# Performance work log

Measured on AMD Instinct MI355X. Metric: run time of the kernel, lower is better.

## Reference

```python
import jax, jax.numpy as jnp
import numpy as np

B, T, D_MODEL, H = 2, 2048, 1024, 16
D_HEAD = D_MODEL // H


def setup_inputs() -> dict:
    key = jax.random.key(0)
    k1, k2, k3 = jax.random.split(key, 3)
    x = jax.random.normal(k1, (B, T, D_MODEL), dtype=jnp.float32)
    # Linear weights stored as (in, out); scale like torch default init roughly
    W_qkv = jax.random.normal(k2, (D_MODEL, 3 * D_MODEL), dtype=jnp.float32) / np.sqrt(D_MODEL)
    W_o = jax.random.normal(k3, (D_MODEL, D_MODEL), dtype=jnp.float32) / np.sqrt(D_MODEL)
    return {"x": x, "W_qkv": W_qkv, "W_o": W_o}


def reference(x, W_qkv, W_o):
    Bx, Tx, C = x.shape
    qkv = x @ W_qkv                                   # (B,T,3C)
    qkv = qkv.reshape(Bx, Tx, 3, H, D_HEAD)
    q = qkv[:, :, 0].transpose(0, 2, 1, 3)            # (B,H,T,D)
    k = qkv[:, :, 1].transpose(0, 2, 1, 3)
    v = qkv[:, :, 2].transpose(0, 2, 1, 3)
    scale = 1.0 / np.sqrt(D_HEAD).astype(np.float32)
    att = jnp.einsum('bhqd,bhkd->bhqk', q, k) * scale  # (B,H,T,T)
    causal = jnp.tril(jnp.ones((Tx, Tx), dtype=bool))
    att = jnp.where(causal[None, None], att, jnp.float32(-jnp.inf))
    w = jax.nn.softmax(att, axis=-1)
    out = jnp.einsum('bhqk,bhkd->bhqd', w, v)          # (B,H,T,D)
    out = out.transpose(0, 2, 1, 3).reshape(Bx, Tx, C)
    return out @ W_o
```

## Files before the change

### kernel.cpp

```cpp
#include <hip/hip_runtime.h>

typedef unsigned short u16;
typedef unsigned int u32;
typedef __bf16 bf16x8 __attribute__((ext_vector_type(8)));
typedef float f32x4 __attribute__((ext_vector_type(4)));

#define DEV __device__ __forceinline__

constexpr int BB = 2;
constexpr int TT = 2048;
constexpr int CD = 1024;
constexpr int HH = 16;
constexpr int DH = 64;
constexpr int BT = BB * TT;

#define QSCALE 0.18033688011112042f

DEV u16 f2bf(float f) {
    return __builtin_bit_cast(u16, (__bf16)f);
}

DEV f32x4 mfma16(bf16x8 a, bf16x8 b, f32x4 c) {
    return __builtin_amdgcn_mfma_f32_16x16x32_bf16(a, b, c, 0, 0, 0);
}

DEV void gld_lds16(u16* lds, const u16* g) {
    __builtin_amdgcn_global_load_lds(
        (const __attribute__((address_space(1))) unsigned int*)g,
        (__attribute__((address_space(3))) unsigned int*)lds, 16, 0, 0);
}

__global__ __launch_bounds__(256)
void prep_kernel(const float* __restrict__ x, u16* __restrict__ xb,
                 const float* __restrict__ Wqkv, u16* __restrict__ WqkvT,
                 const float* __restrict__ Wo, u16* __restrict__ WoT) {
    const int tid = threadIdx.x;
    int blk = blockIdx.x;
    if (blk < 2048) {
        const int i = (blk * 256 + tid) * 8;
        float4 a = *(const float4*)&x[i];
        float4 b = *(const float4*)&x[i + 4];
        u16 t[8];
        t[0] = f2bf(a.x); t[1] = f2bf(a.y); t[2] = f2bf(a.z); t[3] = f2bf(a.w);
        t[4] = f2bf(b.x); t[5] = f2bf(b.y); t[6] = f2bf(b.z); t[7] = f2bf(b.w);
        *(uint4*)&xb[i] = *(const uint4*)t;
        return;
    }
    __shared__ u16 tile[64][72];
    const float* in; u16* out; int rows, cols, bx, by;
    blk -= 2048;
    if (blk < 768) { in = Wqkv; out = WqkvT; rows = 1024; cols = 3072; bx = blk % 48; by = blk / 48; }
    else { blk -= 768; in = Wo; out = WoT; rows = 1024; cols = 1024; bx = blk % 16; by = blk / 16; }
    const int c0 = bx * 64, r0 = by * 64;

    const int tx = tid & 15, ty = tid >> 4;
    #pragma unroll
    for (int p = 0; p < 4; ++p) {
        const int r = ty + p * 16;
        float4 v = *(const float4*)&in[(size_t)(r0 + r) * cols + c0 + tx * 4];
        tile[tx * 4 + 0][r] = f2bf(v.x);
        tile[tx * 4 + 1][r] = f2bf(v.y);
        tile[tx * 4 + 2][r] = f2bf(v.z);
        tile[tx * 4 + 3][r] = f2bf(v.w);
    }
    __syncthreads();

    const int c = tid >> 2, r8 = (tid & 3) * 16;
    u16* dst = &out[(size_t)(c0 + c) * rows + r0 + r8];
    *(uint4*)dst       = *(const uint4*)&tile[c][r8];
    *(uint4*)(dst + 8) = *(const uint4*)&tile[c][r8 + 8];
}

template <int EPI, int BM, int BN, int GX>
__global__ __launch_bounds__(256)
void gemm_db(const u16* __restrict__ A, const u16* __restrict__ Bt,
             u16* __restrict__ out0, u16* __restrict__ out1,
             u16* __restrict__ out2, float* __restrict__ outf,
             int M, int N, int K) {
    constexpr int BK = 32, AST = 32;
    constexpr int MT = BM / 32;
    constexpr int NT = BN / 32;
    constexpr int MBLK = 4096 / BM;
    constexpr int NBLK = GX * MBLK;
    constexpr int CPX = NBLK / 8;
    constexpr int LPS = BM / 64 + BN / 64;
    __shared__ alignas(16) u16 As[3][BM * AST];
    __shared__ alignas(16) u16 Bs[3][BN * AST];

    const int tid  = threadIdx.x;
    const int wave = tid >> 6, lane = tid & 63;
    const int quad = lane >> 4, l16 = lane & 15;
    const int wm = (wave & 1) * (BM / 2), wn = (wave >> 1) * (BN / 2);

    int bid = (int)blockIdx.x;
    bid = (bid & 7) * CPX + (bid >> 3);
    const int bx = bid % GX, by = bid / GX;
    const int m0 = by * BM, n0 = bx * BN;

    const int srowA = wave * (BM / 4) + (lane >> 2);
    const int srowB = wave * (BN / 4) + (lane >> 2);
    const int scol  = (((lane & 3) ^ ((lane >> 3) & 3))) * 8;
    const u16* ga0 = A  + (size_t)(m0 + srowA) * K + scol;
    const u16* ga1 = ga0 + (size_t)16 * K;
    const u16* gb0 = Bt + (size_t)(n0 + srowB) * K + scol;
    const u16* gb1 = gb0 + (size_t)16 * K;

    auto stage = [&](int buf, int k0) {
        gld_lds16(&As[buf][wave * (BM / 4) * 32],       ga0 + k0);
        if constexpr (BM == 128)
            gld_lds16(&As[buf][wave * (BM / 4) * 32 + 512], ga1 + k0);
        gld_lds16(&Bs[buf][wave * (BN / 4) * 32],       gb0 + k0);
        if constexpr (BN == 128)
            gld_lds16(&Bs[buf][wave * (BN / 4) * 32 + 512], gb1 + k0);
    };
    auto wait_lps = [&]() {
        if constexpr (LPS == 4)      asm volatile("s_waitcnt vmcnt(4)" ::: "memory");
        else if constexpr (LPS == 3) asm volatile("s_waitcnt vmcnt(3)" ::: "memory");
        else                         asm volatile("s_waitcnt vmcnt(2)" ::: "memory");
    };

    f32x4 acc[MT][NT] = {};

    stage(0, 0);
    stage(1, BK);
    wait_lps();
    __builtin_amdgcn_s_barrier();

    const int sx = ((l16 >> 1) & 3) * 8;
    const int NS = K / BK;
    int cb = 0;
    for (int t = 0; t < NS; ++t) {
        const bool pf = (t + 2 < NS);
        int sb = cb + 2; if (sb >= 3) sb -= 3;
        if (pf) stage(sb, (t + 2) * BK);

        bf16x8 fa[MT], fb[NT];
        #pragma unroll
        for (int mt = 0; mt < MT; ++mt)
            fa[mt] = *(const bf16x8*)
                &As[cb][(wm + mt * 16 + l16) * AST + (quad * 8 ^ sx)];
        #pragma unroll
        for (int nt = 0; nt < NT; ++nt)
            fb[nt] = *(const bf16x8*)
                &Bs[cb][(wn + nt * 16 + l16) * AST + (quad * 8 ^ sx)];
        #pragma unroll
        for (int mt = 0; mt < MT; ++mt)
            #pragma unroll
            for (int nt = 0; nt < NT; ++nt)
                acc[mt][nt] = mfma16(fa[mt], fb[nt], acc[mt][nt]);

        if (pf) wait_lps();
        else    asm volatile("s_waitcnt vmcnt(0)" ::: "memory");
        __builtin_amdgcn_s_barrier();
        cb = (cb + 1 == 3) ? 0 : cb + 1;
    }

    #pragma unroll
    for (int mt = 0; mt < MT; ++mt) {
        #pragma unroll
        for (int nt = 0; nt < NT; ++nt) {
            #pragma unroll
            for (int reg = 0; reg < 4; ++reg) {
                const int r = m0 + wm + mt * 16 + quad * 4 + reg;
                const int c = n0 + wn + nt * 16 + l16;
                if (EPI == 0) {
                    outf[(size_t)r * N + c] = acc[mt][nt][reg];
                } else {
                    const int which = c >> 10;
                    const int cc = c & 1023;
                    const int h = cc >> 6, d = cc & 63;
                    const int b = r >> 11, t = r & 2047;
                    const int bh = b * HH + h;
                    if (which == 0) {
                        out0[((size_t)bh * TT + t) * DH + d] =
                            f2bf(acc[mt][nt][reg] * QSCALE);
                    } else if (which == 1) {
                        out1[((size_t)bh * TT + t) * DH + d] = f2bf(acc[mt][nt][reg]);
                    } else {
                        out2[((size_t)bh * DH + d) * TT + t] = f2bf(acc[mt][nt][reg]);
                    }
                }
            }
        }
    }
}

constexpr int KST = 72;

DEV void attn_step(const bf16x8 fk[4][2], const bf16x8 fv[2][4],
                   const bf16x8 fone, const bf16x8* fq,
                   f32x4* Oacc, f32x4& lacc, float& m_i, bool diag,
                   int wave, int quad, int l16) {
    f32x4 st[4];
    #pragma unroll
    for (int nt = 0; nt < 4; ++nt) {
        f32x4 t = {};
        t = mfma16(fk[nt][0], fq[0], t);
        t = mfma16(fk[nt][1], fq[1], t);
        st[nt] = t;
    }

    if (diag) {
        const int qg = wave * 16 + l16;
        #pragma unroll
        for (int nt = 0; nt < 4; ++nt)
            #pragma unroll
            for (int reg = 0; reg < 4; ++reg) {
                const int kg = nt * 16 + quad * 4 + reg;
                st[nt][reg] = (kg <= qg) ? st[nt][reg] : -INFINITY;
            }
    }

    float v[16];
    #pragma unroll
    for (int nt = 0; nt < 4; ++nt)
        #pragma unroll
        for (int reg = 0; reg < 4; ++reg)
            v[nt * 4 + reg] = st[nt][reg];
    #pragma unroll
    for (int s = 8; s > 0; s >>= 1)
        #pragma unroll
        for (int i = 0; i < s; ++i)
            v[i] = fmaxf(v[i], v[i + s]);
    float vmax = v[0];
    vmax = fmaxf(vmax, __shfl_xor(vmax, 16, 64));
    vmax = fmaxf(vmax, __shfl_xor(vmax, 32, 64));

    if (!__all(vmax - m_i <= 8.f)) {
        const float mnew = fmaxf(m_i, vmax);
        const float alpha = __builtin_amdgcn_exp2f(m_i - mnew);
        m_i = mnew;
        #pragma unroll
        for (int dt = 0; dt < 4; ++dt)
            #pragma unroll
            for (int reg = 0; reg < 4; ++reg)
                Oacc[dt][reg] *= alpha;
        #pragma unroll
        for (int reg = 0; reg < 4; ++reg)
            lacc[reg] *= alpha;
    }

    #pragma unroll
    for (int nt = 0; nt < 4; ++nt)
        #pragma unroll
        for (int reg = 0; reg < 4; ++reg)
            st[nt][reg] = __builtin_amdgcn_exp2f(st[nt][reg] - m_i);

    #pragma unroll
    for (int pair = 0; pair < 2; ++pair) {
        bf16x8 pb;
        #pragma unroll
        for (int j = 0; j < 4; ++j) {
            pb[j]     = (__bf16)st[2 * pair][j];
            pb[4 + j] = (__bf16)st[2 * pair + 1][j];
        }
        lacc = mfma16(fone, pb, lacc);
        #pragma unroll
        for (int dt = 0; dt < 4; ++dt)
            Oacc[dt] = mfma16(fv[pair][dt], pb, Oacc[dt]);
    }
}

__global__ __launch_bounds__(256, 4)
void attn_kernel(const u16* __restrict__ Q, const u16* __restrict__ Kb,
                 const u16* __restrict__ Vt, u16* __restrict__ O) {
    __shared__ alignas(16) u16 Ks[2][64 * KST];
    __shared__ alignas(16) u16 Vs[2][64 * KST];

    const int bid = (int)blockIdx.x;
    const int j2 = bid >> 3;
    const int qt = 31 - (j2 >> 2);
    const int bh = (bid & 7) + 8 * (j2 & 3);
    const int jmax = qt;

    const int tid = threadIdx.x;
    const int wave = tid >> 6, lane = tid & 63;
    const int quad = lane >> 4, l16 = lane & 15;

    const u16* Qh = Q  + (size_t)bh * TT * DH;
    const u16* Kh = Kb + (size_t)bh * TT * DH;
    const u16* Vh = Vt + (size_t)bh * DH * TT;

    const int row = qt * 64 + wave * 16;

    bf16x8 fq[2];
    fq[0] = *(const bf16x8*)&Qh[(row + l16) * DH + quad * 8];
    fq[1] = *(const bf16x8*)&Qh[(row + l16) * DH + 32 + quad * 8];

    bf16x8 fone;
    {
        const __bf16 ov = (l16 == 0) ? (__bf16)1.f : (__bf16)0.f;
        #pragma unroll
        for (int j = 0; j < 8; ++j) fone[j] = ov;
    }

    f32x4 Oa[4] = {}, lacc = {};
    float m_i = -INFINITY;

    const int trow = tid >> 3;
    const int ic   = tid & 7;
    const int tcol = ic * 8;
    const int vc1 = 32 * (ic >> 2) + 16 * (ic & 1) + 4 * ((ic & 3) >> 1);
    uint4 kr0, kr1, vr0, vr1;

    auto load_chunk = [&](int j) {
        const u16* ks = Kh + (size_t)j * 64 * DH;
        kr0 = *(const uint4*)&ks[trow * DH + tcol];
        kr1 = *(const uint4*)&ks[(trow + 32) * DH + tcol];
        const u16* vs = Vh + (size_t)j * 64;
        vr0 = *(const uint4*)&vs[(size_t)trow * TT + tcol];
        vr1 = *(const uint4*)&vs[(size_t)(trow + 32) * TT + tcol];
    };
    auto write_chunk = [&](int buf) {
        *(uint4*)&Ks[buf][trow * KST + tcol]        = kr0;
        *(uint4*)&Ks[buf][(trow + 32) * KST + tcol] = kr1;
        *(uint2*)&Vs[buf][trow * KST + vc1]            = *(const uint2*)&vr0;
        *(uint2*)&Vs[buf][trow * KST + vc1 + 8]        = *((const uint2*)&vr0 + 1);
        *(uint2*)&Vs[buf][(trow + 32) * KST + vc1]     = *(const uint2*)&vr1;
        *(uint2*)&Vs[buf][(trow + 32) * KST + vc1 + 8] = *((const uint2*)&vr1 + 1);
    };

    load_chunk(0);
    write_chunk(0);

    for (int j = 0; j <= jmax; ++j) {
        const int cur = j & 1;
        __syncthreads();
        if (j < jmax) load_chunk(j + 1);

        bf16x8 fk[4][2], fv[2][4];
        #pragma unroll
        for (int nt = 0; nt < 4; ++nt) {
            fk[nt][0] = *(const bf16x8*)&Ks[cur][(nt * 16 + l16) * KST + quad * 8];
            fk[nt][1] = *(const bf16x8*)&Ks[cur][(nt * 16 + l16) * KST + 32 + quad * 8];
        }
        #pragma unroll
        for (int pair = 0; pair < 2; ++pair)
            #pragma unroll
            for (int dt = 0; dt < 4; ++dt)
                fv[pair][dt] = *(const bf16x8*)
                    &Vs[cur][(dt * 16 + l16) * KST + pair * 32 + quad * 8];

        attn_step(fk, fv, fone, fq, Oa, lacc, m_i, (j == qt),
                  wave, quad, l16);
        if (j < jmax) write_chunk(cur ^ 1);
    }

    const float lrow = __shfl(lacc[0], l16, 64);
    const float r_i = 1.f / lrow;

    const int b = bh >> 4, h = bh & 15;
    #pragma unroll
    for (int dt = 0; dt < 4; ++dt) {
        u16 oa[4];
        #pragma unroll
        for (int reg = 0; reg < 4; ++reg)
            oa[reg] = f2bf(Oa[dt][reg] * r_i);
        *(uint2*)&O[((size_t)(b * TT + row + l16)) * CD + h * DH + dt * 16 + quad * 4] =
            *(const uint2*)oa;
    }
}

extern "C" void kernel_launch(void* const* d_in, const int* in_sizes, int n_in,
                              void* d_out, int out_size, void* d_ws, size_t ws_size,
                              hipStream_t stream) {
    (void)in_sizes; (void)n_in; (void)out_size; (void)ws_size;
    const float* x    = (const float*)d_in[0];
    const float* Wqkv = (const float*)d_in[1];
    const float* Wo   = (const float*)d_in[2];
    float* out = (float*)d_out;

    char* ws = (char*)d_ws;
    u16* xb    = (u16*)(ws + 0);
    u16* WqkvT = (u16*)(ws + (8u  << 20));
    u16* WoT   = (u16*)(ws + (14u << 20));
    u16* Qb    = (u16*)(ws + (16u << 20));
    u16* Kb    = (u16*)(ws + (24u << 20));
    u16* Vt    = (u16*)(ws + (32u << 20));
    u16* attn  = (u16*)(ws + (40u << 20));

    prep_kernel<<<3072, 256, 0, stream>>>(x, xb, Wqkv, WqkvT, Wo, WoT);

    gemm_db<1, 128, 128, 24><<<768, 256, 0, stream>>>(
        xb, WqkvT, Qb, Kb, Vt, nullptr, BT, 3072, CD);

    attn_kernel<<<1024, 256, 0, stream>>>(Qb, Kb, Vt, attn);

    gemm_db<0, 64, 64, 16><<<1024, 256, 0, stream>>>(
        attn, WoT, nullptr, nullptr, nullptr, out, BT, CD, CD);
}
```

Baseline: 175.4 us.

## Split attention query tiles across two blocks and DMA K directly into swizzled LDS

Each 64-row query tile is now handled by two 128-thread blocks of two waves, doubling the grid to 2048 blocks. K chunks are loaded with direct global-to-LDS transfers into an XOR-swizzled unpadded layout, while V is still staged through registers. Double buffering is replaced with a single LDS buffer and a second barrier per iteration. This aims for more blocks in flight and less LDS and register pressure, but it doubles K/V global reads and adds synchronization.

```diff
diff --git a/kernel.cpp b/kernel.cpp
--- a/kernel.cpp
+++ b/kernel.cpp
@@ -190,7 +190,7 @@
 DEV void attn_step(const bf16x8 fk[4][2], const bf16x8 fv[2][4],
                    const bf16x8 fone, const bf16x8* fq,
                    f32x4* Oacc, f32x4& lacc, float& m_i, bool diag,
-                   int wave, int quad, int l16) {
+                   int qg, int quad) {
     f32x4 st[4];
     #pragma unroll
     for (int nt = 0; nt < 4; ++nt) {
@@ -201,7 +201,6 @@
     }
 
     if (diag) {
-        const int qg = wave * 16 + l16;
         #pragma unroll
         for (int nt = 0; nt < 4; ++nt)
             #pragma unroll
@@ -261,16 +260,17 @@
     }
 }
 
-__global__ __launch_bounds__(256, 4)
+__global__ __launch_bounds__(128, 4)
 void attn_kernel(const u16* __restrict__ Q, const u16* __restrict__ Kb,
                  const u16* __restrict__ Vt, u16* __restrict__ O) {
-    __shared__ alignas(16) u16 Ks[2][64 * KST];
-    __shared__ alignas(16) u16 Vs[2][64 * KST];
+    __shared__ alignas(16) u16 Ks[64 * 64];
+    __shared__ alignas(16) u16 Vs[64 * KST];
 
     const int bid = (int)blockIdx.x;
-    const int j2 = bid >> 3;
-    const int qt = 31 - (j2 >> 2);
-    const int bh = (bid & 7) + 8 * (j2 & 3);
+    const int bh = bid & 31;
+    const int t6 = bid >> 5;
+    const int qt = 31 - (t6 >> 1);
+    const int half = t6 & 1;
     const int jmax = qt;
 
     const int tid = threadIdx.x;
@@ -281,7 +281,8 @@
     const u16* Kh = Kb + (size_t)bh * TT * DH;
     const u16* Vh = Vt + (size_t)bh * DH * TT;
 
-    const int row = qt * 64 + wave * 16;
+    const int row = qt * 64 + half * 32 + wave * 16;
+    const int qg  = half * 32 + wave * 16 + l16;
 
     bf16x8 fq[2];
     fq[0] = *(const bf16x8*)&Qh[(row + l16) * DH + quad * 8];
@@ -296,54 +297,63 @@
 
     f32x4 Oa[4] = {}, lacc = {};
     float m_i = -INFINITY;
+
+    const int krow8  = lane >> 3;
+    const int kchunk = ((lane & 7) ^ krow8) * 8;
+    const u16* gK = Kh + (size_t)(wave * 32 + krow8) * DH + kchunk;
+    auto kdma = [&](int j) {
+        const u16* g = gK + (size_t)j * 64 * DH;
+        #pragma unroll
+        for (int i = 0; i < 4; ++i)
+            gld_lds16(&Ks[(wave * 32 + i * 8) * 64], g + (size_t)i * 8 * DH);
+    };
 
     const int trow = tid >> 3;
     const int ic   = tid & 7;
     const int tcol = ic * 8;
     const int vc1 = 32 * (ic >> 2) + 16 * (ic & 1) + 4 * ((ic & 3) >> 1);
-    uint4 kr0, kr1, vr0, vr1;
-
-    auto load_chunk = [&](int j) {
-        const u16* ks = Kh + (size_t)j * 64 * DH;
-        kr0 = *(const uint4*)&ks[trow * DH + tcol];
-        kr1 = *(const uint4*)&ks[(trow + 32) * DH + tcol];
+    uint4 vr[4];
+
+    auto vload = [&](int j) {
         const u16* vs = Vh + (size_t)j * 64;
-        vr0 = *(const uint4*)&vs[(size_t)trow * TT + tcol];
-        vr1 = *(const uint4*)&vs[(size_t)(trow + 32) * TT + tcol];
+        #pragma unroll
+        for (int k = 0; k < 4; ++k)
+            vr[k] = *(const uint4*)&vs[(size_t)(trow + 16 * k) * TT + tcol];
     };
-    auto write_chunk = [&](int buf) {
-        *(uint4*)&Ks[buf][trow * KST + tcol]        = kr0;
-        *(uint4*)&Ks[buf][(trow + 32) * KST + tcol] = kr1;
-        *(uint2*)&Vs[buf][trow * KST + vc1]            = *(const uint2*)&vr0;
-        *(uint2*)&Vs[buf][trow * KST + vc1 + 8]        = *((const uint2*)&vr0 + 1);
-        *(uint2*)&Vs[buf][(trow + 32) * KST + vc1]     = *(const uint2*)&vr1;
-        *(uint2*)&Vs[buf][(trow + 32) * KST + vc1 + 8] = *((const uint2*)&vr1 + 1);
+    auto vwrite = [&]() {
+        #pragma unroll
+        for (int k = 0; k < 4; ++k) {
+            *(uint2*)&Vs[(trow + 16 * k) * KST + vc1]     = *(const uint2*)&vr[k];
+            *(uint2*)&Vs[(trow + 16 * k) * KST + vc1 + 8] = *((const uint2*)&vr[k] + 1);
+        }
     };
 
-    load_chunk(0);
-    write_chunk(0);
+    vload(0);
+    kdma(0);
+    vwrite();
 
     for (int j = 0; j <= jmax; ++j) {
-        const int cur = j & 1;
         __syncthreads();
-        if (j < jmax) load_chunk(j + 1);
+        if (j < jmax) vload(j + 1);
 
         bf16x8 fk[4][2], fv[2][4];
         #pragma unroll
-        for (int nt = 0; nt < 4; ++nt) {
-            fk[nt][0] = *(const bf16x8*)&Ks[cur][(nt * 16 + l16) * KST + quad * 8];
-            fk[nt][1] = *(const bf16x8*)&Ks[cur][(nt * 16 + l16) * KST + 32 + quad * 8];
-        }
+        for (int nt = 0; nt < 4; ++nt)
+            #pragma unroll
+            for (int ks = 0; ks < 2; ++ks)
+                fk[nt][ks] = *(const bf16x8*)
+                    &Ks[(nt * 16 + l16) * 64 + (((ks * 4 + quad) ^ (l16 & 7)) << 3)];
         #pragma unroll
         for (int pair = 0; pair < 2; ++pair)
             #pragma unroll
             for (int dt = 0; dt < 4; ++dt)
                 fv[pair][dt] = *(const bf16x8*)
-                    &Vs[cur][(dt * 16 + l16) * KST + pair * 32 + quad * 8];
-
-        attn_step(fk, fv, fone, fq, Oa, lacc, m_i, (j == qt),
-                  wave, quad, l16);
-        if (j < jmax) write_chunk(cur ^ 1);
+                    &Vs[(dt * 16 + l16) * KST + pair * 32 + quad * 8];
+
+        attn_step(fk, fv, fone, fq, Oa, lacc, m_i, (j == qt), qg, quad);
+
+        __syncthreads();
+        if (j < jmax) { kdma(j + 1); vwrite(); }
     }
 
     const float lrow = __shfl(lacc[0], l16, 64);
@@ -384,7 +394,7 @@
     gemm_db<1, 128, 128, 24><<<768, 256, 0, stream>>>(
         xb, WqkvT, Qb, Kb, Vt, nullptr, BT, 3072, CD);
 
-    attn_kernel<<<1024, 256, 0, stream>>>(Qb, Kb, Vt, attn);
+    attn_kernel<<<2048, 128, 0, stream>>>(Qb, Kb, Vt, attn);
 
     gemm_db<0, 64, 64, 16><<<1024, 256, 0, stream>>>(
         attn, WoT, nullptr, nullptr, nullptr, out, BT, CD, CD);
```

Result: slower. 181.2 us (+3.3%).
